# Optimization experiments

Measured on AMD Instinct MI355X. Metric: run time of the kernel, lower is better.

## Reference

```python
import jax, jax.numpy as jnp
import numpy as np

N_NODES = 100000
N_EDGES = 1600000
IN_CH = 128
HEADS = 4
HEAD_DIM = 16  # out_channels // heads = 64 // 4
EPS = 1e-8
NEG_SLOPE = 0.2


def setup_inputs() -> dict:
    key = jax.random.key(0)
    k1, k2, k3, k4, k5 = jax.random.split(key, 5)
    x = jax.random.normal(k1, (N_NODES, IN_CH), dtype=jnp.float32)
    edge_index = jax.random.randint(k2, (2, N_EDGES), 0, N_NODES, dtype=jnp.int64)
    edge_weight = jax.random.uniform(k3, (N_EDGES,), dtype=jnp.float32)
    # Linear(in_channels, heads*head_dim, bias=False): weight [out, in]
    W = jax.random.normal(k4, (HEADS * HEAD_DIM, IN_CH), dtype=jnp.float32) * 0.05
    a = jax.random.normal(k5, (1, HEADS, 2 * HEAD_DIM), dtype=jnp.float32) * 0.1
    return {"x": x, "edge_index": edge_index, "edge_weight": edge_weight, "W": W, "a": a}


def reference(x, edge_index, edge_weight, W, a):
    num_nodes = x.shape[0]
    h = (x @ W.T).reshape(num_nodes, HEADS, HEAD_DIM)  # [N, H, D]
    src, dst = edge_index[0], edge_index[1]
    h_src = h[src]  # [E, H, D]
    h_dst = h[dst]  # [E, H, D]
    # a * concat(h_src, h_dst) summed over last dim == split-dot (avoids concat)
    a_src = a[..., :HEAD_DIM]  # [1, H, D]
    a_dst = a[..., HEAD_DIM:]  # [1, H, D]
    attention = jnp.sum(a_src * h_src + a_dst * h_dst, axis=-1)  # [E, H]
    attention = jax.nn.leaky_relu(attention, negative_slope=NEG_SLOPE)
    attention = attention * edge_weight[:, None]
    attention = jnp.exp(attention)
    att_sum = jax.ops.segment_sum(attention, dst, num_segments=num_nodes)  # [N, H]
    attention = attention / (att_sum[dst] + EPS)  # [E, H]
    # dropout is identity in eval mode
    weighted = h_src * attention[:, :, None]  # [E, H, D]
    out = jax.ops.segment_sum(weighted, dst, num_segments=num_nodes)  # [N, H, D]
    return out.reshape(num_nodes, HEADS * HEAD_DIM)
```

## Files before the change

kernel.cpp:

```cpp
#include <hip/hip_runtime.h>
#include <math.h>

#define N_NODES 100000
#define N_EDGES 1600000
#define IN_CH 128
#define HEADS 4
#define HEAD_DIM 16
#define OUT_CH 64
#define NEG_SLOPE 0.2f
#define EPS 1e-8f

#define NBUCK 391
#define NBLK1 512
#define CHUNK (N_EDGES / NBLK1)
#define CAPG 4608
#define CAP CAPG
#define GEMM_BLOCKS ((N_NODES + 127) / 128)
#define FAT_BLOCKS (NBLK1 + GEMM_BLOCKS)

typedef _Float16 f16x8 __attribute__((ext_vector_type(8)));
typedef _Float16 f16x4 __attribute__((ext_vector_type(4)));
typedef float    f32x4 __attribute__((ext_vector_type(4)));

#define SWZ(b) ((b) ^ ((((b) >> 8) & 7) << 4))

__device__ inline f16x8 cvt8(const float* p) {
    float4 lo = ((const float4*)p)[0];
    float4 hi = ((const float4*)p)[1];
    f16x8 f;
    f[0] = (_Float16)lo.x; f[1] = (_Float16)lo.y;
    f[2] = (_Float16)lo.z; f[3] = (_Float16)lo.w;
    f[4] = (_Float16)hi.x; f[5] = (_Float16)hi.y;
    f[6] = (_Float16)hi.z; f[7] = (_Float16)hi.w;
    return f;
}

__global__ __launch_bounds__(512, 6) void gemm_scatter_kernel(
    const float* __restrict__ x,
    const float* __restrict__ W,
    const float* __restrict__ a,
    const int* __restrict__ ei,
    const float* __restrict__ ew,
    int* __restrict__ gcur,
    unsigned long long* __restrict__ tmp,
    _Float16* __restrict__ h,
    float* __restrict__ alpha_src,
    float* __restrict__ alpha_dst)
{
    __shared__ __align__(16) char smem[36864];

    if (blockIdx.x < NBLK1) {
        int* cnt  = (int*)smem;
        int* dbuf = (int*)(smem + 1664);
        for (int j = threadIdx.x; j < NBUCK; j += 512) cnt[j] = 0;
        __syncthreads();
        const int base = blockIdx.x * CHUNK;
        for (int i = threadIdx.x; i < CHUNK; i += 512) {
            int d = ei[N_EDGES + base + i];
            dbuf[i] = d;
            atomicAdd(&cnt[d >> 8], 1);
        }
        __syncthreads();
        for (int j = threadIdx.x; j < NBUCK; j += 512) {
            int c = cnt[j];
            int b = (c > 0) ? atomicAdd(&gcur[j], c) : 0;
            cnt[j] = j * CAPG + b;
        }
        __syncthreads();
        for (int i = threadIdx.x; i < CHUNK; i += 512) {
            int e = base + i;
            int d = dbuf[i];
            int s = ei[e];
            float w = ew[e];
            int pos = atomicAdd(&cnt[d >> 8], 1);
            unsigned long long pk = ((unsigned long long)__float_as_uint(w) << 32)
                                  | ((unsigned)(d & 255) << 17) | (unsigned)s;
            tmp[pos] = pk;
        }
    } else {
        _Float16* whs = (_Float16*)smem;
        _Float16* hst = (_Float16*)(smem + 18432);

        const int gb = blockIdx.x - NBLK1;
        const int wv = threadIdx.x >> 6;
        const int lane = threadIdx.x & 63;
        const int col = lane & 15;
        const int quad = lane >> 4;

        for (int i = threadIdx.x; i < 1024; i += 512) {
            int row = i >> 4, koff = (i & 15) << 3;
            int b = (row << 8) + (koff << 1);
            *(f16x8*)((char*)whs + SWZ(b)) = cvt8(W + row * IN_CH + koff);
        }
        for (int i = threadIdx.x; i < 1024; i += 512) {
            int r8 = i >> 7, k = i & 127;
            int hd = r8 & 3, half = r8 >> 2;
            const float* av = a + hd * 32 + half * 16;
            const float* wb = W + hd * 16 * IN_CH + k;
            float s = 0.f;
#pragma unroll
            for (int c = 0; c < 16; c++)
                s += av[c] * wb[c * IN_CH];
            int b = ((64 + r8) << 8) + (k << 1);
            *(_Float16*)((char*)whs + SWZ(b)) = (_Float16)s;
        }
        __syncthreads();

        const int node_base = gb * 128 + wv * 16;
        int row_node = node_base + col;
        int rn = row_node < N_NODES ? row_node : N_NODES - 1;
        const float* xrow = x + (long long)rn * IN_CH;

        f16x8 afrag[4];
#pragma unroll
        for (int ks = 0; ks < 4; ks++)
            afrag[ks] = cvt8(xrow + ks * 32 + quad * 8);

        f32x4 acc[5];
#pragma unroll
        for (int nt = 0; nt < 5; nt++) {
            f32x4 z = {0.f, 0.f, 0.f, 0.f};
            acc[nt] = z;
        }

#pragma unroll
        for (int ks = 0; ks < 4; ks++) {
#pragma unroll
            for (int nt = 0; nt < 5; nt++) {
                int r = (nt < 4) ? nt * 16 + col : 64 + (col & 7);
                int b = (r << 8) + (ks << 6) + (quad << 4);
                f16x8 bf = *(const f16x8*)((const char*)whs + SWZ(b));
                if (nt == 4 && col >= 8) {
                    f16x8 z = {};
                    bf = z;
                }
                acc[nt] = __builtin_amdgcn_mfma_f32_16x16x32_f16(
                    afrag[ks], bf, acc[nt], 0, 0, 0);
            }
        }

#pragma unroll
        for (int r = 0; r < 4; r++) {
            int nl = wv * 16 + quad * 4 + r;
#pragma unroll
            for (int nt = 0; nt < 4; nt++)
                hst[nl * 72 + nt * 16 + col] = (_Float16)acc[nt][r];
            int node = node_base + quad * 4 + r;
            if (node < N_NODES) {
                if (col < 4)      alpha_src[node * HEADS + col]     = acc[4][r];
                else if (col < 8) alpha_dst[node * HEADS + col - 4] = acc[4][r];
            }
        }

        __syncthreads();
        const int bnode = gb * 128;
        const int nrem = N_NODES - bnode;
        const int climit = (nrem < 128 ? nrem : 128) << 3;
        for (int i = threadIdx.x; i < 1024; i += 512) {
            if (i < climit) {
                int node = i >> 3, ch8 = i & 7;
                *(f16x8*)(h + (long long)(bnode + node) * OUT_CH + ch8 * 8) =
                    *(const f16x8*)&hst[node * 72 + ch8 * 8];
            }
        }
    }
}

__global__ __launch_bounds__(512) void finalize_kernel(
    const unsigned long long* __restrict__ tmp,
    const int* __restrict__ gcur,
    long long* __restrict__ csr, int* __restrict__ ptr)
{
    __shared__ int cnt[256];
    __shared__ int offs[256];
    __shared__ int scanbuf[512];
    __shared__ unsigned short rk[CAP];
    __shared__ unsigned long long stage[CAP];
    const int j = blockIdx.x;
    const int t = threadIdx.x;

    int gv = (t < NBUCK) ? gcur[t] : 0;
    scanbuf[t] = gv;
    if (t < 256) cnt[t] = 0;
    __syncthreads();
    for (int off = 1; off < 512; off <<= 1) {
        int xx = (t >= off) ? scanbuf[t - off] : 0;
        __syncthreads();
        scanbuf[t] += xx;
        __syncthreads();
    }
    const int incl = scanbuf[j];
    const int beg  = (j > 0) ? scanbuf[j - 1] : 0;
    const int len  = incl - beg;
    if (j == 0 && t == 0) ptr[N_NODES] = N_EDGES;
    const unsigned long long* src = tmp + (size_t)j * CAPG;

    for (int i = t; i < len; i += 512) {
        unsigned long long pk = __builtin_nontemporal_load(&src[i]);
        stage[i] = pk;
        rk[i] = (unsigned short)atomicAdd(&cnt[(int)((pk >> 17) & 255)], 1);
    }
    __syncthreads();
    int v = (t < 256) ? cnt[t] : 0;
    for (int off = 1; off < 256; off <<= 1) {
        int xx = (t < 256 && t >= off) ? cnt[t - off] : 0;
        __syncthreads();
        if (t < 256) cnt[t] += xx;
        __syncthreads();
    }
    if (t < 256) {
        int excl = cnt[t] - v;
        int node = j * 256 + t;
        if (node < N_NODES) ptr[node] = beg + excl;
        offs[t] = excl;
    }
    __syncthreads();
    for (int i = t; i < len; i += 512) {
        unsigned long long pk = stage[i];
        int dloc = (int)((pk >> 17) & 255);
        int pos = offs[dloc] + (int)rk[i];
        unsigned long long vv = (pk & 0xFFFFFFFF00000000ull) | (pk & 0x1FFFFull);
        ((unsigned long long*)csr)[beg + pos] = vv;
    }
}

__global__ __launch_bounds__(256) void aggregate_kernel(
    const int* __restrict__ ptr,
    const int2* __restrict__ csr,
    const float4* __restrict__ alpha_src4,
    const float4* __restrict__ alpha_dst4,
    const _Float16* __restrict__ h,
    float* __restrict__ out)
{
    __shared__ float4 sev[4][64];
    __shared__ int    ssc[4][64];

    const int wv = threadIdx.x >> 6;
    const int lane = threadIdx.x & 63;
    const int n = blockIdx.x * 4 + wv;
    if (n >= N_NODES) return;
    const int q = lane >> 4;
    const int cg = lane & 15;
    const int hsel = cg >> 2;

    const int beg = ptr[n];
    const int end = ptr[n + 1];
    const float4 ad4 = alpha_dst4[n];

    float4 acc = make_float4(0.f, 0.f, 0.f, 0.f);
    float denom = 0.f;
    float4* sev_w = sev[wv];
    int* ssc_w = ssc[wv];

    for (int base = beg; base < end; base += 64) {
        int cnt = min(64, end - base);
        int s_l = 0;
        float4 e4 = make_float4(0.f, 0.f, 0.f, 0.f);
        if (lane < cnt) {
            int2 pr = csr[base + lane];
            s_l = pr.x;
            float w = __int_as_float(pr.y);
            float4 as = alpha_src4[s_l];
            float t0 = as.x + ad4.x; t0 = (t0 > 0.f ? t0 : NEG_SLOPE * t0) * w;
            float t1 = as.y + ad4.y; t1 = (t1 > 0.f ? t1 : NEG_SLOPE * t1) * w;
            float t2 = as.z + ad4.z; t2 = (t2 > 0.f ? t2 : NEG_SLOPE * t2) * w;
            float t3 = as.w + ad4.w; t3 = (t3 > 0.f ? t3 : NEG_SLOPE * t3) * w;
            e4 = make_float4(__expf(t0), __expf(t1), __expf(t2), __expf(t3));
        }
        sev_w[lane] = e4;
        ssc_w[lane] = s_l;

        int iters = (cnt + 3) >> 2;
        for (int j0 = 0; j0 < iters; j0 += 2) {
            int idx0 = j0 * 4 + q;
            int idx1 = idx0 + 4;
            int s0 = ssc_w[idx0];
            int s1 = ssc_w[idx1];
            float ev0 = ((const float*)&sev_w[idx0])[hsel];
            float ev1 = ((const float*)&sev_w[idx1])[hsel];
            f16x4 h0 = *(const f16x4*)(h + s0 * OUT_CH + cg * 4);
            f16x4 h1 = *(const f16x4*)(h + s1 * OUT_CH + cg * 4);
            acc.x += ev0 * (float)h0[0] + ev1 * (float)h1[0];
            acc.y += ev0 * (float)h0[1] + ev1 * (float)h1[1];
            acc.z += ev0 * (float)h0[2] + ev1 * (float)h1[2];
            acc.w += ev0 * (float)h0[3] + ev1 * (float)h1[3];
            denom += ev0 + ev1;
        }
    }

    denom += __shfl_xor(denom, 16);
    denom += __shfl_xor(denom, 32);
    acc.x += __shfl_xor(acc.x, 16);  acc.x += __shfl_xor(acc.x, 32);
    acc.y += __shfl_xor(acc.y, 16);  acc.y += __shfl_xor(acc.y, 32);
    acc.z += __shfl_xor(acc.z, 16);  acc.z += __shfl_xor(acc.z, 32);
    acc.w += __shfl_xor(acc.w, 16);  acc.w += __shfl_xor(acc.w, 32);

    if (lane < 16) {
        float inv = 1.f / (denom + EPS);
        float4 r = make_float4(acc.x * inv, acc.y * inv, acc.z * inv, acc.w * inv);
        ((float4*)(out + (long long)n * OUT_CH))[cg] = r;
    }
}

extern "C" void kernel_launch(void* const* d_in, const int* in_sizes, int n_in,
                              void* d_out, int out_size, void* d_ws, size_t ws_size,
                              hipStream_t stream) {
    const float* x  = (const float*)d_in[0];
    const int*   ei = (const int*)d_in[1];
    const float* ew = (const float*)d_in[2];
    const float* W  = (const float*)d_in[3];
    const float* a  = (const float*)d_in[4];
    float* out = (float*)d_out;

    char* p = (char*)d_ws;
    _Float16* h      = (_Float16*)p; p += (size_t)N_NODES * OUT_CH * 2;
    float* alpha_src = (float*)p;  p += (size_t)N_NODES * HEADS * 4;
    float* alpha_dst = (float*)p;  p += (size_t)N_NODES * HEADS * 4;
    int*   gcur      = (int*)p;    p += (size_t)400 * 4;
    int*   ptr       = (int*)p;    p += (size_t)(N_NODES + 4) * 4;
    unsigned long long* tmp = (unsigned long long*)p;
    p += (size_t)NBUCK * CAPG * 8;
    long long* csr   = (long long*)p;

    hipMemsetAsync(gcur, 0, 400 * sizeof(int), stream);

    gemm_scatter_kernel<<<FAT_BLOCKS, 512, 0, stream>>>(
        x, W, a, ei, ew, gcur, tmp, h, alpha_src, alpha_dst);
    finalize_kernel<<<NBUCK, 512, 0, stream>>>(tmp, gcur, csr, ptr);
    aggregate_kernel<<<(N_NODES + 3) / 4, 256, 0, stream>>>(
        ptr, (const int2*)csr, (const float4*)alpha_src, (const float4*)alpha_dst, h, out);
}
```

Measured before the change: 193.0 us.

## Fuse CSR finalize into aggregation using per-bucket shared-memory grouping

Removes the separate finalize kernel that built a global CSR and ptr array, and instead has each block take half of a 256-node destination bucket. The block counts, scans and groups that half's edges in shared memory, then aggregates directly from there. This drops one kernel launch and the global CSR write and read-back. In exchange, each block reads its bucket's tmp data twice, and only 782 blocks of 512 threads are launched versus 25000 small blocks before, so load balance and occupancy may suffer. Edges beyond CAPH per half-bucket are silently dropped.

```diff
diff --git a/kernel.cpp b/kernel.cpp
--- a/kernel.cpp
+++ b/kernel.cpp
@@ -14,7 +14,7 @@
 #define NBLK1 512
 #define CHUNK (N_EDGES / NBLK1)
 #define CAPG 4608
-#define CAP CAPG
+#define CAPH 2560
 #define GEMM_BLOCKS ((N_NODES + 127) / 128)
 #define FAT_BLOCKS (NBLK1 + GEMM_BLOCKS)
 
@@ -166,139 +166,122 @@
     }
 }
 
-__global__ __launch_bounds__(512) void finalize_kernel(
+__global__ __launch_bounds__(512) void group_aggregate_kernel(
     const unsigned long long* __restrict__ tmp,
     const int* __restrict__ gcur,
-    long long* __restrict__ csr, int* __restrict__ ptr)
-{
-    __shared__ int cnt[256];
-    __shared__ int offs[256];
-    __shared__ int scanbuf[512];
-    __shared__ unsigned short rk[CAP];
-    __shared__ unsigned long long stage[CAP];
-    const int j = blockIdx.x;
-    const int t = threadIdx.x;
-
-    int gv = (t < NBUCK) ? gcur[t] : 0;
-    scanbuf[t] = gv;
-    if (t < 256) cnt[t] = 0;
-    __syncthreads();
-    for (int off = 1; off < 512; off <<= 1) {
-        int xx = (t >= off) ? scanbuf[t - off] : 0;
-        __syncthreads();
-        scanbuf[t] += xx;
-        __syncthreads();
-    }
-    const int incl = scanbuf[j];
-    const int beg  = (j > 0) ? scanbuf[j - 1] : 0;
-    const int len  = incl - beg;
-    if (j == 0 && t == 0) ptr[N_NODES] = N_EDGES;
-    const unsigned long long* src = tmp + (size_t)j * CAPG;
-
-    for (int i = t; i < len; i += 512) {
-        unsigned long long pk = __builtin_nontemporal_load(&src[i]);
-        stage[i] = pk;
-        rk[i] = (unsigned short)atomicAdd(&cnt[(int)((pk >> 17) & 255)], 1);
-    }
-    __syncthreads();
-    int v = (t < 256) ? cnt[t] : 0;
-    for (int off = 1; off < 256; off <<= 1) {
-        int xx = (t < 256 && t >= off) ? cnt[t - off] : 0;
-        __syncthreads();
-        if (t < 256) cnt[t] += xx;
-        __syncthreads();
-    }
-    if (t < 256) {
-        int excl = cnt[t] - v;
-        int node = j * 256 + t;
-        if (node < N_NODES) ptr[node] = beg + excl;
-        offs[t] = excl;
-    }
-    __syncthreads();
-    for (int i = t; i < len; i += 512) {
-        unsigned long long pk = stage[i];
-        int dloc = (int)((pk >> 17) & 255);
-        int pos = offs[dloc] + (int)rk[i];
-        unsigned long long vv = (pk & 0xFFFFFFFF00000000ull) | (pk & 0x1FFFFull);
-        ((unsigned long long*)csr)[beg + pos] = vv;
-    }
-}
-
-__global__ __launch_bounds__(256) void aggregate_kernel(
-    const int* __restrict__ ptr,
-    const int2* __restrict__ csr,
     const float4* __restrict__ alpha_src4,
     const float4* __restrict__ alpha_dst4,
     const _Float16* __restrict__ h,
     float* __restrict__ out)
 {
-    __shared__ float4 sev[4][64];
-    __shared__ int    ssc[4][64];
-
-    const int wv = threadIdx.x >> 6;
-    const int lane = threadIdx.x & 63;
-    const int n = blockIdx.x * 4 + wv;
-    if (n >= N_NODES) return;
+    __shared__ int cntA[128];
+    __shared__ int baseA[128];
+    __shared__ int curA[128];
+    __shared__ unsigned long long grouped[CAPH];
+    __shared__ float4 sev[8][64];
+    __shared__ int    ssc[8][64];
+
+    const int j = blockIdx.x >> 1;
+    const int half = blockIdx.x & 1;
+    const int t = threadIdx.x;
+    const int len = min(gcur[j], CAPG);
+    const unsigned long long* src = tmp + (size_t)j * CAPG;
+
+    if (t < 128) cntA[t] = 0;
+    __syncthreads();
+
+    for (int i = t; i < len; i += 512) {
+        int dloc = (int)((src[i] >> 17) & 255);
+        if ((dloc >> 7) == half) atomicAdd(&cntA[dloc & 127], 1);
+    }
+    __syncthreads();
+    if (t < 128) curA[t] = cntA[t];
+    __syncthreads();
+    for (int off = 1; off < 128; off <<= 1) {
+        int xx = (t < 128 && t >= off) ? curA[t - off] : 0;
+        __syncthreads();
+        if (t < 128) curA[t] += xx;
+        __syncthreads();
+    }
+    if (t < 128) { baseA[t] = curA[t] - cntA[t]; curA[t] = baseA[t]; }
+    __syncthreads();
+    for (int i = t; i < len; i += 512) {
+        unsigned long long pk = src[i];
+        int dloc = (int)((pk >> 17) & 255);
+        if ((dloc >> 7) == half) {
+            int pos = atomicAdd(&curA[dloc & 127], 1);
+            if (pos < CAPH) grouped[pos] = pk;
+        }
+    }
+    __syncthreads();
+
+    const int wv = t >> 6;
+    const int lane = t & 63;
     const int q = lane >> 4;
     const int cg = lane & 15;
     const int hsel = cg >> 2;
-
-    const int beg = ptr[n];
-    const int end = ptr[n + 1];
-    const float4 ad4 = alpha_dst4[n];
-
-    float4 acc = make_float4(0.f, 0.f, 0.f, 0.f);
-    float denom = 0.f;
     float4* sev_w = sev[wv];
     int* ssc_w = ssc[wv];
 
-    for (int base = beg; base < end; base += 64) {
-        int cnt = min(64, end - base);
-        int s_l = 0;
-        float4 e4 = make_float4(0.f, 0.f, 0.f, 0.f);
-        if (lane < cnt) {
-            int2 pr = csr[base + lane];
-            s_l = pr.x;
-            float w = __int_as_float(pr.y);
-            float4 as = alpha_src4[s_l];
-            float t0 = as.x + ad4.x; t0 = (t0 > 0.f ? t0 : NEG_SLOPE * t0) * w;
-            float t1 = as.y + ad4.y; t1 = (t1 > 0.f ? t1 : NEG_SLOPE * t1) * w;
-            float t2 = as.z + ad4.z; t2 = (t2 > 0.f ? t2 : NEG_SLOPE * t2) * w;
-            float t3 = as.w + ad4.w; t3 = (t3 > 0.f ? t3 : NEG_SLOPE * t3) * w;
-            e4 = make_float4(__expf(t0), __expf(t1), __expf(t2), __expf(t3));
-        }
-        sev_w[lane] = e4;
-        ssc_w[lane] = s_l;
-
-        int iters = (cnt + 3) >> 2;
-        for (int j0 = 0; j0 < iters; j0 += 2) {
-            int idx0 = j0 * 4 + q;
-            int idx1 = idx0 + 4;
-            int s0 = ssc_w[idx0];
-            int s1 = ssc_w[idx1];
-            float ev0 = ((const float*)&sev_w[idx0])[hsel];
-            float ev1 = ((const float*)&sev_w[idx1])[hsel];
-            f16x4 h0 = *(const f16x4*)(h + s0 * OUT_CH + cg * 4);
-            f16x4 h1 = *(const f16x4*)(h + s1 * OUT_CH + cg * 4);
-            acc.x += ev0 * (float)h0[0] + ev1 * (float)h1[0];
-            acc.y += ev0 * (float)h0[1] + ev1 * (float)h1[1];
-            acc.z += ev0 * (float)h0[2] + ev1 * (float)h1[2];
-            acc.w += ev0 * (float)h0[3] + ev1 * (float)h1[3];
-            denom += ev0 + ev1;
-        }
-    }
-
-    denom += __shfl_xor(denom, 16);
-    denom += __shfl_xor(denom, 32);
-    acc.x += __shfl_xor(acc.x, 16);  acc.x += __shfl_xor(acc.x, 32);
-    acc.y += __shfl_xor(acc.y, 16);  acc.y += __shfl_xor(acc.y, 32);
-    acc.z += __shfl_xor(acc.z, 16);  acc.z += __shfl_xor(acc.z, 32);
-    acc.w += __shfl_xor(acc.w, 16);  acc.w += __shfl_xor(acc.w, 32);
-
-    if (lane < 16) {
-        float inv = 1.f / (denom + EPS);
-        float4 r = make_float4(acc.x * inv, acc.y * inv, acc.z * inv, acc.w * inv);
-        ((float4*)(out + (long long)n * OUT_CH))[cg] = r;
+    for (int nl = wv; nl < 128; nl += 8) {
+        int n = j * 256 + half * 128 + nl;
+        if (n >= N_NODES) continue;
+        int ebeg = baseA[nl];
+        int deg = cntA[nl];
+        if (ebeg + deg > CAPH) deg = (CAPH > ebeg) ? CAPH - ebeg : 0;
+        const float4 ad4 = alpha_dst4[n];
+
+        float4 acc = make_float4(0.f, 0.f, 0.f, 0.f);
+        float denom = 0.f;
+
+        for (int b0 = 0; b0 < deg; b0 += 64) {
+            int cnt_e = min(64, deg - b0);
+            int s_l = 0;
+            float4 e4 = make_float4(0.f, 0.f, 0.f, 0.f);
+            if (lane < cnt_e) {
+                unsigned long long pk = grouped[ebeg + b0 + lane];
+                s_l = (int)(pk & 0x1FFFF);
+                float w = __int_as_float((int)(pk >> 32));
+                float4 as = alpha_src4[s_l];
+                float t0 = as.x + ad4.x; t0 = (t0 > 0.f ? t0 : NEG_SLOPE * t0) * w;
+                float t1 = as.y + ad4.y; t1 = (t1 > 0.f ? t1 : NEG_SLOPE * t1) * w;
+                float t2 = as.z + ad4.z; t2 = (t2 > 0.f ? t2 : NEG_SLOPE * t2) * w;
+                float t3 = as.w + ad4.w; t3 = (t3 > 0.f ? t3 : NEG_SLOPE * t3) * w;
+                e4 = make_float4(__expf(t0), __expf(t1), __expf(t2), __expf(t3));
+            }
+            sev_w[lane] = e4;
+            ssc_w[lane] = s_l;
+
+            int iters = (cnt_e + 3) >> 2;
+            for (int j0 = 0; j0 < iters; j0 += 2) {
+                int idx0 = j0 * 4 + q;
+                int idx1 = idx0 + 4;
+                int s0 = ssc_w[idx0];
+                int s1 = ssc_w[idx1];
+                float ev0 = ((const float*)&sev_w[idx0])[hsel];
+                float ev1 = ((const float*)&sev_w[idx1])[hsel];
+                f16x4 h0 = *(const f16x4*)(h + s0 * OUT_CH + cg * 4);
+                f16x4 h1 = *(const f16x4*)(h + s1 * OUT_CH + cg * 4);
+                acc.x += ev0 * (float)h0[0] + ev1 * (float)h1[0];
+                acc.y += ev0 * (float)h0[1] + ev1 * (float)h1[1];
+                acc.z += ev0 * (float)h0[2] + ev1 * (float)h1[2];
+                acc.w += ev0 * (float)h0[3] + ev1 * (float)h1[3];
+                denom += ev0 + ev1;
+            }
+        }
+
+        denom += __shfl_xor(denom, 16);
+        denom += __shfl_xor(denom, 32);
+        acc.x += __shfl_xor(acc.x, 16);  acc.x += __shfl_xor(acc.x, 32);
+        acc.y += __shfl_xor(acc.y, 16);  acc.y += __shfl_xor(acc.y, 32);
+        acc.z += __shfl_xor(acc.z, 16);  acc.z += __shfl_xor(acc.z, 32);
+        acc.w += __shfl_xor(acc.w, 16);  acc.w += __shfl_xor(acc.w, 32);
+
+        if (lane < 16) {
+            float inv = 1.f / (denom + EPS);
+            float4 r = make_float4(acc.x * inv, acc.y * inv, acc.z * inv, acc.w * inv);
+            ((float4*)(out + (long long)n * OUT_CH))[cg] = r;
+        }
     }
 }
 
@@ -317,16 +300,12 @@
     float* alpha_src = (float*)p;  p += (size_t)N_NODES * HEADS * 4;
     float* alpha_dst = (float*)p;  p += (size_t)N_NODES * HEADS * 4;
     int*   gcur      = (int*)p;    p += (size_t)400 * 4;
-    int*   ptr       = (int*)p;    p += (size_t)(N_NODES + 4) * 4;
     unsigned long long* tmp = (unsigned long long*)p;
-    p += (size_t)NBUCK * CAPG * 8;
-    long long* csr   = (long long*)p;
 
     hipMemsetAsync(gcur, 0, 400 * sizeof(int), stream);
 
     gemm_scatter_kernel<<<FAT_BLOCKS, 512, 0, stream>>>(
         x, W, a, ei, ew, gcur, tmp, h, alpha_src, alpha_dst);
-    finalize_kernel<<<NBUCK, 512, 0, stream>>>(tmp, gcur, csr, ptr);
-    aggregate_kernel<<<(N_NODES + 3) / 4, 256, 0, stream>>>(
-        ptr, (const int2*)csr, (const float4*)alpha_src, (const float4*)alpha_dst, h, out);
+    group_aggregate_kernel<<<NBUCK * 2, 512, 0, stream>>>(
+        tmp, gcur, (const float4*)alpha_src, (const float4*)alpha_dst, h, out);
 }
```

Measured after the change: 191.5 us. No clear change (-0.8%).
